# Kernel tuning notes

Measured on AMD Instinct MI355X. Metric: run time of the kernel, lower is better.

## Reference

```python
import jax, jax.numpy as jnp
import numpy as np

N_LVL = 127.0   # 8-bit symmetric: 2**(8-1) - 1
BN_EPS = 1e-5
PATCH = 16


def quant_act(x):
    """Per-tensor 8-bit symmetric quant-dequant (HAWQ-style QuantAct, dynamic range)."""
    scale = jnp.max(jnp.abs(x)) / N_LVL
    xq = jnp.clip(jnp.round(x / scale), -N_LVL, N_LVL) * scale
    return xq, scale


def setup_inputs() -> dict:
    key = jax.random.key(0)
    k0, k1, k2, k3, k4 = jax.random.split(key, 5)
    B, C, H = 128, 3, 224
    dim = 768
    x = jax.random.normal(k0, (B, C, H, H), jnp.float32)
    W = jax.random.normal(k1, (dim, C, PATCH, PATCH), jnp.float32) * 0.02
    b = jax.random.normal(k2, (dim,), jnp.float32) * 0.02
    gamma = jnp.ones((dim,), jnp.float32)
    beta = jnp.zeros((dim,), jnp.float32)
    run_mean = jax.random.normal(k3, (dim,), jnp.float32) * 0.1
    run_var = jax.random.uniform(k4, (dim,), jnp.float32, 0.5, 1.5)
    return {"x": x, "W": W, "b": b, "gamma": gamma, "beta": beta,
            "run_mean": run_mean, "run_var": run_var}


def reference(x, W, b, gamma, beta, run_mean, run_var):
    # --- quant_input ---
    x_q, pre_s = quant_act(x)                                   # [B,3,224,224], scalar
    # --- QuantConv2d: per-out-channel 8-bit symmetric weight quant ---
    w_scale = jnp.max(jnp.abs(W), axis=(1, 2, 3), keepdims=True) / N_LVL  # [dim,1,1,1]
    w_int = jnp.round(W / w_scale)
    x_int = x_q / pre_s                                         # integer-valued activations
    comb_s = w_scale[:, 0, 0, 0] * pre_s                        # [dim] conv output scale
    b_int = jnp.round(b / comb_s)
    y = jax.lax.conv_general_dilated(
        x_int, w_int, window_strides=(PATCH, PATCH), padding='VALID',
        dimension_numbers=('NCHW', 'OIHW', 'NCHW'))             # [B,768,14,14]
    y = (y + b_int[None, :, None, None]) * comb_s[None, :, None, None]
    # --- quant_act_conv ---
    y, _ = quant_act(y)
    # --- GELU (torch nn.GELU default: exact erf) ---
    y = jax.nn.gelu(y, approximate=False)
    # --- qact1 ---
    y, _ = quant_act(y)
    # --- BatchNorm2d (eval mode, running stats) ---
    inv = gamma / jnp.sqrt(run_var + BN_EPS)
    y = y * inv[None, :, None, None] + (beta - run_mean * inv)[None, :, None, None]
    # --- qact2 ---
    y, act_scale = quant_act(y)
    return y, act_scale
```

## Files before the change

kernel.cpp:

```cpp
#include <hip/hip_runtime.h>

#define TOT   19267584
#define MROWS 25088
#define KD    768
#define NPB   196
#define CHW   150528

typedef unsigned int uint;
typedef __attribute__((ext_vector_type(4))) int i32x4;

#define OFF_AQ   0ull
#define OFF_WQ   19267584ull
#define OFF_WSC  19857408ull
#define OFF_INV  19860480ull
#define OFF_SHF  19863552ull
#define OFF_PA   19866624ull
#define OFF_PB   19871328ull
#define OFF_CMN  19876032ull
#define OFF_CMX  19879104ull

__device__ __forceinline__ float wave_max(float v) {
#pragma unroll
  for (int off = 32; off > 0; off >>= 1) v = fmaxf(v, __shfl_xor(v, off));
  return v;
}

__device__ __forceinline__ float block_max(float v) {
  __shared__ float red[4];
  v = wave_max(v);
  __syncthreads();
  if ((threadIdx.x & 63) == 0) red[threadIdx.x >> 6] = v;
  __syncthreads();
  return fmaxf(fmaxf(red[0], red[1]), fmaxf(red[2], red[3]));
}

__global__ void k_maxabs(const float* __restrict__ x, float* __restrict__ pA) {
  const int i0 = blockIdx.x * 256 + threadIdx.x;
  const float4* x4 = (const float4*)x;
  float m = 0.f;
#pragma unroll
  for (int j = 0; j < 16; j += 4) {
    float4 a = x4[i0 + (j + 0) * 301056];
    float4 b = x4[i0 + (j + 1) * 301056];
    float4 c = x4[i0 + (j + 2) * 301056];
    float4 d = x4[i0 + (j + 3) * 301056];
    m = fmaxf(m, fmaxf(fmaxf(fabsf(a.x), fabsf(a.y)), fmaxf(fabsf(a.z), fabsf(a.w))));
    m = fmaxf(m, fmaxf(fmaxf(fabsf(b.x), fabsf(b.y)), fmaxf(fabsf(b.z), fabsf(b.w))));
    m = fmaxf(m, fmaxf(fmaxf(fabsf(c.x), fabsf(c.y)), fmaxf(fabsf(c.z), fabsf(c.w))));
    m = fmaxf(m, fmaxf(fmaxf(fabsf(d.x), fabsf(d.y)), fmaxf(fabsf(d.z), fabsf(d.w))));
  }
  float bm = block_max(m);
  if (threadIdx.x == 0) pA[blockIdx.x] = bm;
}

__global__ void k_wquant(const float* __restrict__ W, const float* __restrict__ gamma,
                         const float* __restrict__ beta, const float* __restrict__ rmean,
                         const float* __restrict__ rvar, signed char* __restrict__ wq,
                         float* __restrict__ wscale, float* __restrict__ inv_,
                         float* __restrict__ shf) {
  const int oc = blockIdx.x;
  const float* row = W + oc * KD;
  float m = 0.f;
  for (int k = threadIdx.x; k < KD; k += 256) m = fmaxf(m, fabsf(row[k]));
  const float ws_ = block_max(m) / 127.0f;
  for (int k = threadIdx.x; k < KD; k += 256)
    wq[oc * KD + k] = (signed char)(int)rintf(row[k] / ws_);
  if (threadIdx.x == 0) {
    wscale[oc] = ws_;
    float iv = gamma[oc] / sqrtf(rvar[oc] + 1e-5f);
    inv_[oc] = iv;
    shf[oc] = __fsub_rn(beta[oc], __fmul_rn(rmean[oc], iv));
  }
}

__global__ void k_im2col(const float* __restrict__ x, const float* __restrict__ pA,
                         signed char* __restrict__ aq) {
  float mm = 0.f;
  for (int i = threadIdx.x; i < 1176; i += 256) mm = fmaxf(mm, pA[i]);
  const float ps = block_max(mm) / 127.0f;
  const int u = blockIdx.x * 256 + threadIdx.x;
  const int p = u / 48, r = u - p * 48;
  const int c = r >> 4, kh = r & 15;
  const int b = p / NPB, pp = p - b * NPB;
  const int ph = pp / 14, pw = pp - ph * 14;
  const float* src = x + (((b * 3 + c) * 224 + ph * 16 + kh) * 224 + pw * 16);
  float4 v0 = *(const float4*)(src);
  float4 v1 = *(const float4*)(src + 4);
  float4 v2 = *(const float4*)(src + 8);
  float4 v3 = *(const float4*)(src + 12);
#define Q8(v) ((int)fminf(fmaxf(rintf((v) / ps), -127.f), 127.f) & 255)
  uint4 o;
  o.x = Q8(v0.x) | (Q8(v0.y) << 8) | (Q8(v0.z) << 16) | ((uint)Q8(v0.w) << 24);
  o.y = Q8(v1.x) | (Q8(v1.y) << 8) | (Q8(v1.z) << 16) | ((uint)Q8(v1.w) << 24);
  o.z = Q8(v2.x) | (Q8(v2.y) << 8) | (Q8(v2.z) << 16) | ((uint)Q8(v2.w) << 24);
  o.w = Q8(v3.x) | (Q8(v3.y) << 8) | (Q8(v3.z) << 16) | ((uint)Q8(v3.w) << 24);
#undef Q8
  *(uint4*)(aq + (size_t)p * KD + (r << 4)) = o;
}

__device__ __forceinline__ void gl_lds16(const void* g, void* l) {
  __builtin_amdgcn_global_load_lds((const __attribute__((address_space(1))) void*)g,
                                   (__attribute__((address_space(3))) void*)l, 16, 0, 0);
}

__global__ __launch_bounds__(256) void k_gemm(const signed char* __restrict__ aq,
                                              const signed char* __restrict__ wq,
                                              const float* __restrict__ bias,
                                              const float* __restrict__ wscale,
                                              const float* __restrict__ pA,
                                              float* __restrict__ y,
                                              float* __restrict__ pB) {
  __shared__ __align__(16) signed char lA[3][8192];
  __shared__ __align__(16) signed char lB[3][8192];
  const int tid = threadIdx.x, lane = tid & 63, wv = tid >> 6;
  const int bsw = (blockIdx.x & 7) * 147 + (blockIdx.x >> 3);
  const int bm = bsw / 6, bn = bsw - 6 * (bsw / 6);
  const int wr = wv >> 1, wc = wv & 1;

  const int ci0 = wv * 2, ci1 = wv * 2 + 1;
  const int rr0 = ci0 * 16 + (lane >> 2);
  const int rr1 = ci1 * 16 + (lane >> 2);
  const int bo = (((lane & 3) ^ ((lane >> 3) & 3)) << 4);
  const signed char* gA0 = aq + (size_t)(bm * 128 + rr0) * KD + bo;
  const signed char* gA1 = aq + (size_t)(bm * 128 + rr1) * KD + bo;
  const signed char* gB0 = wq + (size_t)(bn * 128 + rr0) * KD + bo;
  const signed char* gB1 = wq + (size_t)(bn * 128 + rr1) * KD + bo;

  i32x4 acc[4][4];
#pragma unroll
  for (int m = 0; m < 4; ++m)
#pragma unroll
    for (int n = 0; n < 4; ++n) acc[m][n] = (i32x4){0, 0, 0, 0};

  const int rbase = lane & 15;
  const int kg = (((lane >> 4) << 4)) ^ (((lane >> 1) & 3) << 4);

#define STAGE(T, B)                                   \
  {                                                   \
    const int kk_ = (T) * 64;                         \
    gl_lds16(gA0 + kk_, &lA[B][ci0 * 1024]);          \
    gl_lds16(gA1 + kk_, &lA[B][ci1 * 1024]);          \
    gl_lds16(gB0 + kk_, &lB[B][ci0 * 1024]);          \
    gl_lds16(gB1 + kk_, &lB[B][ci1 * 1024]);          \
  }

  STAGE(0, 0)
  STAGE(1, 1)
#pragma unroll
  for (int t = 0; t < 12; ++t) {
    if (t < 11) { asm volatile("s_waitcnt vmcnt(4)" ::: "memory"); }
    else        { asm volatile("s_waitcnt vmcnt(0)" ::: "memory"); }
    __builtin_amdgcn_s_barrier();
    __builtin_amdgcn_sched_barrier(0);
    const int b = t % 3;
    i32x4 af[4], bfr[4];
#pragma unroll
    for (int m = 0; m < 4; ++m)
      af[m] = *(const i32x4*)&lA[b][(wr * 64 + m * 16 + rbase) * 64 + kg];
#pragma unroll
    for (int n = 0; n < 4; ++n)
      bfr[n] = *(const i32x4*)&lB[b][(wc * 64 + n * 16 + rbase) * 64 + kg];
    if (t < 10) STAGE(t + 2, (t + 2) % 3)
#pragma unroll
    for (int m = 0; m < 4; ++m)
#pragma unroll
      for (int n = 0; n < 4; ++n)
        acc[m][n] = __builtin_amdgcn_mfma_i32_16x16x64_i8(af[m], bfr[n], acc[m][n], 0, 0, 0);
  }
#undef STAGE

  float mm = 0.f;
  for (int i = tid; i < 1176; i += 256) mm = fmaxf(mm, pA[i]);
  const float ps = block_max(mm) / 127.0f;

  float lmax = 0.f;
  const int prow = (lane >> 4) << 2;
#pragma unroll
  for (int n = 0; n < 4; ++n) {
    const int oc = bn * 128 + wc * 64 + n * 16 + rbase;
    const float comb = wscale[oc] * ps;
    const float bint = rintf(bias[oc] / comb);
#pragma unroll
    for (int m = 0; m < 4; ++m) {
      const int p0 = bm * 128 + wr * 64 + m * 16 + prow;
      const int img = p0 / 196;
      const int q = p0 - img * 196;
      float4 o;
      o.x = ((float)acc[m][n][0] + bint) * comb;
      o.y = ((float)acc[m][n][1] + bint) * comb;
      o.z = ((float)acc[m][n][2] + bint) * comb;
      o.w = ((float)acc[m][n][3] + bint) * comb;
      lmax = fmaxf(lmax, fmaxf(fmaxf(fabsf(o.x), fabsf(o.y)), fmaxf(fabsf(o.z), fabsf(o.w))));
      *(float4*)(y + (size_t)img * CHW + (size_t)oc * 196 + q) = o;
    }
  }
  float bm_ = block_max(lmax);
  if (tid == 0) pB[blockIdx.x] = bm_;
}

__global__ void k_gelu_chan(const float* __restrict__ y, const float* __restrict__ pB,
                            signed char* __restrict__ k1, float* __restrict__ chmn,
                            float* __restrict__ chmx) {
  const int c = blockIdx.x;
  float mm = 0.f;
  for (int i = threadIdx.x; i < 1176; i += 256) mm = fmaxf(mm, pB[i]);
  const float s1 = block_max(mm) / 127.0f;
  __shared__ float tab[255];
  for (int t = threadIdx.x; t < 255; t += 256) {
    float y1 = (float)(t - 127) * s1;
    float e = erff(y1 * 0.70710678118654752f);
    tab[t] = (y1 * (e + 1.0f)) * 0.5f;
  }
  __syncthreads();
  float mn = 1e30f, mx = -1e30f;
  const float4* y4 = (const float4*)y;
  char4* k4 = (char4*)k1;
#define ADDR(u) ((size_t)((u) / 49) * (CHW / 4) + (size_t)c * 49 + ((u) - ((u) / 49) * 49))
#define PROC(v, a4)                                                        \
  {                                                                        \
    int ia = (int)fminf(fmaxf(rintf((v).x / s1), -127.f), 127.f);          \
    int ib = (int)fminf(fmaxf(rintf((v).y / s1), -127.f), 127.f);          \
    int ic = (int)fminf(fmaxf(rintf((v).z / s1), -127.f), 127.f);          \
    int id = (int)fminf(fmaxf(rintf((v).w / s1), -127.f), 127.f);          \
    char4 kk;                                                              \
    kk.x = (signed char)ia; kk.y = (signed char)ib;                        \
    kk.z = (signed char)ic; kk.w = (signed char)id;                        \
    k4[a4] = kk;                                                           \
    float ga = tab[ia + 127], gb = tab[ib + 127];                          \
    float gc = tab[ic + 127], gd = tab[id + 127];                          \
    mn = fminf(mn, fminf(fminf(ga, gb), fminf(gc, gd)));                   \
    mx = fmaxf(mx, fmaxf(fmaxf(ga, gb), fmaxf(gc, gd)));                   \
  }
  for (int r = 0; r < 6; ++r) {
    const int u0 = threadIdx.x + r * 1024;
    const size_t a0 = ADDR(u0), a1 = ADDR(u0 + 256), a2 = ADDR(u0 + 512), a3 = ADDR(u0 + 768);
    float4 v0 = y4[a0];
    float4 v1 = y4[a1];
    float4 v2 = y4[a2];
    float4 v3 = y4[a3];
    PROC(v0, a0) PROC(v1, a1) PROC(v2, a2) PROC(v3, a3)
  }
  if (threadIdx.x < 128) {
    const int u = 6144 + threadIdx.x;
    const size_t a = ADDR(u);
    float4 v = y4[a];
    PROC(v, a)
  }
#undef PROC
#undef ADDR
  __shared__ float rmn[4], rmx[4];
#pragma unroll
  for (int off = 32; off > 0; off >>= 1) {
    mn = fminf(mn, __shfl_xor(mn, off));
    mx = fmaxf(mx, __shfl_xor(mx, off));
  }
  const int lane = threadIdx.x & 63, wvx = threadIdx.x >> 6;
  if (lane == 0) { rmn[wvx] = mn; rmx[wvx] = mx; }
  __syncthreads();
  if (threadIdx.x == 0) {
    chmn[c] = fminf(fminf(rmn[0], rmn[1]), fminf(rmn[2], rmn[3]));
    chmx[c] = fmaxf(fmaxf(rmx[0], rmx[1]), fmaxf(rmx[2], rmx[3]));
  }
}

__global__ void k_final(const signed char* __restrict__ k1, const float* __restrict__ pB,
                        const float* __restrict__ chmn, const float* __restrict__ chmx,
                        const float* __restrict__ inv_, const float* __restrict__ shf,
                        float* __restrict__ out) {
  float mm = 0.f;
  for (int i = threadIdx.x; i < 1176; i += 256) mm = fmaxf(mm, pB[i]);
  const float s1 = block_max(mm) / 127.0f;
  float m2 = 0.f;
  for (int c = threadIdx.x; c < 768; c += 256)
    m2 = fmaxf(m2, fmaxf(fabsf(chmn[c]), fabsf(chmx[c])));
  const float s2 = block_max(m2) / 127.0f;
  float m4 = 0.f;
  for (int c = threadIdx.x; c < 768; c += 256) {
    float iv = inv_[c], sh = shf[c];
    float a = fminf(fmaxf(rintf(chmn[c] / s2), -127.f), 127.f) * s2;
    float b = fminf(fmaxf(rintf(chmx[c] / s2), -127.f), 127.f) * s2;
    float ya = __fadd_rn(__fmul_rn(a, iv), sh);
    float yb = __fadd_rn(__fmul_rn(b, iv), sh);
    m4 = fmaxf(m4, fmaxf(fabsf(ya), fabsf(yb)));
  }
  const float s3 = block_max(m4) / 127.0f;

  __shared__ float tab[255];
  for (int t = threadIdx.x; t < 255; t += 256) {
    float y1 = (float)(t - 127) * s1;
    float e = erff(y1 * 0.70710678118654752f);
    float y2 = (y1 * (e + 1.0f)) * 0.5f;
    float q2 = fminf(fmaxf(rintf(y2 / s2), -127.f), 127.f);
    tab[t] = q2 * s2;
  }
  __syncthreads();
  const int i = blockIdx.x * 256 + threadIdx.x;
  const char4* k4 = (const char4*)k1;
  char4 a0 = k4[i];
  char4 a1 = k4[i + 1204224];
  char4 a2 = k4[i + 2 * 1204224];
  char4 a3 = k4[i + 3 * 1204224];
  float4* out4 = (float4*)out;
#define FIN(kk, idx)                                                       \
  {                                                                        \
    int c = ((idx) / 49) % 768;                                            \
    float iv = inv_[c], sh = shf[c];                                       \
    float fa = __fadd_rn(__fmul_rn(tab[kk.x + 127], iv), sh);              \
    float fb = __fadd_rn(__fmul_rn(tab[kk.y + 127], iv), sh);              \
    float fc = __fadd_rn(__fmul_rn(tab[kk.z + 127], iv), sh);              \
    float fd = __fadd_rn(__fmul_rn(tab[kk.w + 127], iv), sh);              \
    float4 o;                                                              \
    o.x = fminf(fmaxf(rintf(fa / s3), -127.f), 127.f) * s3;                \
    o.y = fminf(fmaxf(rintf(fb / s3), -127.f), 127.f) * s3;                \
    o.z = fminf(fmaxf(rintf(fc / s3), -127.f), 127.f) * s3;                \
    o.w = fminf(fmaxf(rintf(fd / s3), -127.f), 127.f) * s3;                \
    out4[idx] = o;                                                         \
  }
  FIN(a0, i)
  FIN(a1, i + 1204224)
  FIN(a2, i + 2 * 1204224)
  FIN(a3, i + 3 * 1204224)
#undef FIN
  if (blockIdx.x == 0 && threadIdx.x == 0) out[TOT] = s3;
}

extern "C" void kernel_launch(void* const* d_in, const int* in_sizes, int n_in,
                              void* d_out, int out_size, void* d_ws, size_t ws_size,
                              hipStream_t stream) {
  const float* x     = (const float*)d_in[0];
  const float* W     = (const float*)d_in[1];
  const float* bias  = (const float*)d_in[2];
  const float* gamma = (const float*)d_in[3];
  const float* beta  = (const float*)d_in[4];
  const float* rmean = (const float*)d_in[5];
  const float* rvar  = (const float*)d_in[6];
  float* out = (float*)d_out;
  char* ws = (char*)d_ws;

  signed char* aq  = (signed char*)(ws + OFF_AQ);
  signed char* wq  = (signed char*)(ws + OFF_WQ);
  float* wsc  = (float*)(ws + OFF_WSC);
  float* inv_ = (float*)(ws + OFF_INV);
  float* shf  = (float*)(ws + OFF_SHF);
  float* pA   = (float*)(ws + OFF_PA);
  float* pB   = (float*)(ws + OFF_PB);
  float* cmn  = (float*)(ws + OFF_CMN);
  float* cmx  = (float*)(ws + OFF_CMX);
  signed char* k1 = (signed char*)(ws + OFF_AQ);

  k_maxabs<<<1176, 256, 0, stream>>>(x, pA);
  k_wquant<<<768, 256, 0, stream>>>(W, gamma, beta, rmean, rvar, wq, wsc, inv_, shf);
  k_im2col<<<4704, 256, 0, stream>>>(x, pA, aq);
  k_gemm<<<1176, 256, 0, stream>>>(aq, wq, bias, wsc, pA, out, pB);
  k_gelu_chan<<<768, 256, 0, stream>>>(out, pB, k1, cmn, cmx);
  k_final<<<4704, 256, 0, stream>>>(k1, pB, cmn, cmx, inv_, shf, out);
}
```

Before: 125.6 us.

## Merge prologue kernels, halve GEMM M-tile, split per-channel GELU blocks

The input max-abs and weight-quant kernels become one launch with block-index dispatch, which saves a launch and lets the two run side by side. The GEMM tile shrinks from 128x128 to 64x128, giving 2352 blocks from one shared LDS buffer of three stages, to even out work across CUs. Each GELU per-channel block is split into two halves over the batch, with per-half min/max combined in the final kernel. Each GEMM block now does less MFMA work per byte loaded and the partial-max arrays get longer, so reuse drops and per-block overhead rises.

```diff
diff --git a/kernel.cpp b/kernel.cpp
--- a/kernel.cpp
+++ b/kernel.cpp
@@ -16,8 +16,8 @@
 #define OFF_SHF  19863552ull
 #define OFF_PA   19866624ull
 #define OFF_PB   19871328ull
-#define OFF_CMN  19876032ull
-#define OFF_CMX  19879104ull
+#define OFF_CMN  19880736ull
+#define OFF_CMX  19886880ull
 
 __device__ __forceinline__ float wave_max(float v) {
 #pragma unroll
@@ -34,42 +34,43 @@
   return fmaxf(fmaxf(red[0], red[1]), fmaxf(red[2], red[3]));
 }
 
-__global__ void k_maxabs(const float* __restrict__ x, float* __restrict__ pA) {
-  const int i0 = blockIdx.x * 256 + threadIdx.x;
-  const float4* x4 = (const float4*)x;
-  float m = 0.f;
-#pragma unroll
-  for (int j = 0; j < 16; j += 4) {
-    float4 a = x4[i0 + (j + 0) * 301056];
-    float4 b = x4[i0 + (j + 1) * 301056];
-    float4 c = x4[i0 + (j + 2) * 301056];
-    float4 d = x4[i0 + (j + 3) * 301056];
-    m = fmaxf(m, fmaxf(fmaxf(fabsf(a.x), fabsf(a.y)), fmaxf(fabsf(a.z), fabsf(a.w))));
-    m = fmaxf(m, fmaxf(fmaxf(fabsf(b.x), fabsf(b.y)), fmaxf(fabsf(b.z), fabsf(b.w))));
-    m = fmaxf(m, fmaxf(fmaxf(fabsf(c.x), fabsf(c.y)), fmaxf(fabsf(c.z), fabsf(c.w))));
-    m = fmaxf(m, fmaxf(fmaxf(fabsf(d.x), fabsf(d.y)), fmaxf(fabsf(d.z), fabsf(d.w))));
-  }
-  float bm = block_max(m);
-  if (threadIdx.x == 0) pA[blockIdx.x] = bm;
-}
-
-__global__ void k_wquant(const float* __restrict__ W, const float* __restrict__ gamma,
+__global__ void k_max_wq(const float* __restrict__ x, float* __restrict__ pA,
+                         const float* __restrict__ W, const float* __restrict__ gamma,
                          const float* __restrict__ beta, const float* __restrict__ rmean,
                          const float* __restrict__ rvar, signed char* __restrict__ wq,
                          float* __restrict__ wscale, float* __restrict__ inv_,
                          float* __restrict__ shf) {
-  const int oc = blockIdx.x;
-  const float* row = W + oc * KD;
-  float m = 0.f;
-  for (int k = threadIdx.x; k < KD; k += 256) m = fmaxf(m, fabsf(row[k]));
-  const float ws_ = block_max(m) / 127.0f;
-  for (int k = threadIdx.x; k < KD; k += 256)
-    wq[oc * KD + k] = (signed char)(int)rintf(row[k] / ws_);
-  if (threadIdx.x == 0) {
-    wscale[oc] = ws_;
-    float iv = gamma[oc] / sqrtf(rvar[oc] + 1e-5f);
-    inv_[oc] = iv;
-    shf[oc] = __fsub_rn(beta[oc], __fmul_rn(rmean[oc], iv));
+  if (blockIdx.x < 1176) {
+    const int i0 = blockIdx.x * 256 + threadIdx.x;
+    const float4* x4 = (const float4*)x;
+    float m = 0.f;
+#pragma unroll
+    for (int j = 0; j < 16; j += 4) {
+      float4 a = x4[i0 + (j + 0) * 301056];
+      float4 b = x4[i0 + (j + 1) * 301056];
+      float4 c = x4[i0 + (j + 2) * 301056];
+      float4 d = x4[i0 + (j + 3) * 301056];
+      m = fmaxf(m, fmaxf(fmaxf(fabsf(a.x), fabsf(a.y)), fmaxf(fabsf(a.z), fabsf(a.w))));
+      m = fmaxf(m, fmaxf(fmaxf(fabsf(b.x), fabsf(b.y)), fmaxf(fabsf(b.z), fabsf(b.w))));
+      m = fmaxf(m, fmaxf(fmaxf(fabsf(c.x), fabsf(c.y)), fmaxf(fabsf(c.z), fabsf(c.w))));
+      m = fmaxf(m, fmaxf(fmaxf(fabsf(d.x), fabsf(d.y)), fmaxf(fabsf(d.z), fabsf(d.w))));
+    }
+    float bm = block_max(m);
+    if (threadIdx.x == 0) pA[blockIdx.x] = bm;
+  } else {
+    const int oc = blockIdx.x - 1176;
+    const float* row = W + oc * KD;
+    float m = 0.f;
+    for (int k = threadIdx.x; k < KD; k += 256) m = fmaxf(m, fabsf(row[k]));
+    const float ws_ = block_max(m) / 127.0f;
+    for (int k = threadIdx.x; k < KD; k += 256)
+      wq[oc * KD + k] = (signed char)(int)rintf(row[k] / ws_);
+    if (threadIdx.x == 0) {
+      wscale[oc] = ws_;
+      float iv = gamma[oc] / sqrtf(rvar[oc] + 1e-5f);
+      inv_[oc] = iv;
+      shf[oc] = __fsub_rn(beta[oc], __fmul_rn(rmean[oc], iv));
+    }
   }
 }
 
@@ -110,59 +111,57 @@
                                               const float* __restrict__ pA,
                                               float* __restrict__ y,
                                               float* __restrict__ pB) {
-  __shared__ __align__(16) signed char lA[3][8192];
-  __shared__ __align__(16) signed char lB[3][8192];
+  __shared__ __align__(16) signed char L[3][12288];
   const int tid = threadIdx.x, lane = tid & 63, wv = tid >> 6;
-  const int bsw = (blockIdx.x & 7) * 147 + (blockIdx.x >> 3);
+  const int bsw = (blockIdx.x & 7) * 294 + (blockIdx.x >> 3);
   const int bm = bsw / 6, bn = bsw - 6 * (bsw / 6);
   const int wr = wv >> 1, wc = wv & 1;
 
-  const int ci0 = wv * 2, ci1 = wv * 2 + 1;
-  const int rr0 = ci0 * 16 + (lane >> 2);
-  const int rr1 = ci1 * 16 + (lane >> 2);
   const int bo = (((lane & 3) ^ ((lane >> 3) & 3)) << 4);
-  const signed char* gA0 = aq + (size_t)(bm * 128 + rr0) * KD + bo;
-  const signed char* gA1 = aq + (size_t)(bm * 128 + rr1) * KD + bo;
-  const signed char* gB0 = wq + (size_t)(bn * 128 + rr0) * KD + bo;
-  const signed char* gB1 = wq + (size_t)(bn * 128 + rr1) * KD + bo;
-
-  i32x4 acc[4][4];
-#pragma unroll
-  for (int m = 0; m < 4; ++m)
+#define SRC(c) ((c) < 4 ? aq + (size_t)(bm * 64 + (c) * 16 + (lane >> 2)) * KD + bo \
+                        : wq + (size_t)(bn * 128 + ((c) - 4) * 16 + (lane >> 2)) * KD + bo)
+  const int c0 = wv * 3, c1 = wv * 3 + 1, c2 = wv * 3 + 2;
+  const signed char* g0 = SRC(c0);
+  const signed char* g1 = SRC(c1);
+  const signed char* g2 = SRC(c2);
+#undef SRC
+
+  i32x4 acc[2][4];
+#pragma unroll
+  for (int m = 0; m < 2; ++m)
 #pragma unroll
     for (int n = 0; n < 4; ++n) acc[m][n] = (i32x4){0, 0, 0, 0};
 
   const int rbase = lane & 15;
-  const int kg = (((lane >> 4) << 4)) ^ (((lane >> 1) & 3) << 4);
+  const int kg = ((lane >> 4) << 4) ^ (((lane >> 1) & 3) << 4);
 
 #define STAGE(T, B)                                   \
   {                                                   \
     const int kk_ = (T) * 64;                         \
-    gl_lds16(gA0 + kk_, &lA[B][ci0 * 1024]);          \
-    gl_lds16(gA1 + kk_, &lA[B][ci1 * 1024]);          \
-    gl_lds16(gB0 + kk_, &lB[B][ci0 * 1024]);          \
-    gl_lds16(gB1 + kk_, &lB[B][ci1 * 1024]);          \
+    gl_lds16(g0 + kk_, &L[B][c0 * 1024]);             \
+    gl_lds16(g1 + kk_, &L[B][c1 * 1024]);             \
+    gl_lds16(g2 + kk_, &L[B][c2 * 1024]);             \
   }
 
   STAGE(0, 0)
   STAGE(1, 1)
 #pragma unroll
   for (int t = 0; t < 12; ++t) {
-    if (t < 11) { asm volatile("s_waitcnt vmcnt(4)" ::: "memory"); }
+    if (t < 11) { asm volatile("s_waitcnt vmcnt(3)" ::: "memory"); }
     else        { asm volatile("s_waitcnt vmcnt(0)" ::: "memory"); }
     __builtin_amdgcn_s_barrier();
     __builtin_amdgcn_sched_barrier(0);
     const int b = t % 3;
-    i32x4 af[4], bfr[4];
-#pragma unroll
-    for (int m = 0; m < 4; ++m)
-      af[m] = *(const i32x4*)&lA[b][(wr * 64 + m * 16 + rbase) * 64 + kg];
+    i32x4 af[2], bfr[4];
+#pragma unroll
+    for (int m = 0; m < 2; ++m)
+      af[m] = *(const i32x4*)&L[b][(wr * 32 + m * 16 + rbase) * 64 + kg];
 #pragma unroll
     for (int n = 0; n < 4; ++n)
-      bfr[n] = *(const i32x4*)&lB[b][(wc * 64 + n * 16 + rbase) * 64 + kg];
+      bfr[n] = *(const i32x4*)&L[b][4096 + (wc * 64 + n * 16 + rbase) * 64 + kg];
     if (t < 10) STAGE(t + 2, (t + 2) % 3)
 #pragma unroll
-    for (int m = 0; m < 4; ++m)
+    for (int m = 0; m < 2; ++m)
 #pragma unroll
       for (int n = 0; n < 4; ++n)
         acc[m][n] = __builtin_amdgcn_mfma_i32_16x16x64_i8(af[m], bfr[n], acc[m][n], 0, 0, 0);
@@ -181,8 +180,8 @@
     const float comb = wscale[oc] * ps;
     const float bint = rintf(bias[oc] / comb);
 #pragma unroll
-    for (int m = 0; m < 4; ++m) {
-      const int p0 = bm * 128 + wr * 64 + m * 16 + prow;
+    for (int m = 0; m < 2; ++m) {
+      const int p0 = bm * 64 + wr * 32 + m * 16 + prow;
       const int img = p0 / 196;
       const int q = p0 - img * 196;
       float4 o;
@@ -199,11 +198,11 @@
 }
 
 __global__ void k_gelu_chan(const float* __restrict__ y, const float* __restrict__ pB,
-                            signed char* __restrict__ k1, float* __restrict__ chmn,
-                            float* __restrict__ chmx) {
-  const int c = blockIdx.x;
+                            signed char* __restrict__ k1, float* __restrict__ cmn2,
+                            float* __restrict__ cmx2) {
+  const int c = blockIdx.x >> 1, half = blockIdx.x & 1;
   float mm = 0.f;
-  for (int i = threadIdx.x; i < 1176; i += 256) mm = fmaxf(mm, pB[i]);
+  for (int i = threadIdx.x; i < 2352; i += 256) mm = fmaxf(mm, pB[i]);
   const float s1 = block_max(mm) / 127.0f;
   __shared__ float tab[255];
   for (int t = threadIdx.x; t < 255; t += 256) {
@@ -215,7 +214,7 @@
   float mn = 1e30f, mx = -1e30f;
   const float4* y4 = (const float4*)y;
   char4* k4 = (char4*)k1;
-#define ADDR(u) ((size_t)((u) / 49) * (CHW / 4) + (size_t)c * 49 + ((u) - ((u) / 49) * 49))
+#define ADDR(u) ((size_t)(half * 64 + (u) / 49) * (CHW / 4) + (size_t)c * 49 + ((u) - ((u) / 49) * 49))
 #define PROC(v, a4)                                                        \
   {                                                                        \
     int ia = (int)fminf(fmaxf(rintf((v).x / s1), -127.f), 127.f);          \
@@ -231,7 +230,7 @@
     mn = fminf(mn, fminf(fminf(ga, gb), fminf(gc, gd)));                   \
     mx = fmaxf(mx, fmaxf(fmaxf(ga, gb), fmaxf(gc, gd)));                   \
   }
-  for (int r = 0; r < 6; ++r) {
+  for (int r = 0; r < 3; ++r) {
     const int u0 = threadIdx.x + r * 1024;
     const size_t a0 = ADDR(u0), a1 = ADDR(u0 + 256), a2 = ADDR(u0 + 512), a3 = ADDR(u0 + 768);
     float4 v0 = y4[a0];
@@ -240,8 +239,8 @@
     float4 v3 = y4[a3];
     PROC(v0, a0) PROC(v1, a1) PROC(v2, a2) PROC(v3, a3)
   }
-  if (threadIdx.x < 128) {
-    const int u = 6144 + threadIdx.x;
+  if (threadIdx.x < 64) {
+    const int u = 3072 + threadIdx.x;
     const size_t a = ADDR(u);
     float4 v = y4[a];
     PROC(v, a)
@@ -258,27 +257,29 @@
   if (lane == 0) { rmn[wvx] = mn; rmx[wvx] = mx; }
   __syncthreads();
   if (threadIdx.x == 0) {
-    chmn[c] = fminf(fminf(rmn[0], rmn[1]), fminf(rmn[2], rmn[3]));
-    chmx[c] = fmaxf(fmaxf(rmx[0], rmx[1]), fmaxf(rmx[2], rmx[3]));
+    cmn2[blockIdx.x] = fminf(fminf(rmn[0], rmn[1]), fminf(rmn[2], rmn[3]));
+    cmx2[blockIdx.x] = fmaxf(fmaxf(rmx[0], rmx[1]), fmaxf(rmx[2], rmx[3]));
   }
 }
 
 __global__ void k_final(const signed char* __restrict__ k1, const float* __restrict__ pB,
-                        const float* __restrict__ chmn, const float* __restrict__ chmx,
+                        const float* __restrict__ cmn2, const float* __restrict__ cmx2,
                         const float* __restrict__ inv_, const float* __restrict__ shf,
                         float* __restrict__ out) {
   float mm = 0.f;
-  for (int i = threadIdx.x; i < 1176; i += 256) mm = fmaxf(mm, pB[i]);
+  for (int i = threadIdx.x; i < 2352; i += 256) mm = fmaxf(mm, pB[i]);
   const float s1 = block_max(mm) / 127.0f;
   float m2 = 0.f;
-  for (int c = threadIdx.x; c < 768; c += 256)
-    m2 = fmaxf(m2, fmaxf(fabsf(chmn[c]), fabsf(chmx[c])));
+  for (int i = threadIdx.x; i < 1536; i += 256)
+    m2 = fmaxf(m2, fmaxf(fabsf(cmn2[i]), fabsf(cmx2[i])));
   const float s2 = block_max(m2) / 127.0f;
   float m4 = 0.f;
   for (int c = threadIdx.x; c < 768; c += 256) {
+    float mn = fminf(cmn2[2 * c], cmn2[2 * c + 1]);
+    float mx = fmaxf(cmx2[2 * c], cmx2[2 * c + 1]);
     float iv = inv_[c], sh = shf[c];
-    float a = fminf(fmaxf(rintf(chmn[c] / s2), -127.f), 127.f) * s2;
-    float b = fminf(fmaxf(rintf(chmx[c] / s2), -127.f), 127.f) * s2;
+    float a = fminf(fmaxf(rintf(mn / s2), -127.f), 127.f) * s2;
+    float b = fminf(fmaxf(rintf(mx / s2), -127.f), 127.f) * s2;
     float ya = __fadd_rn(__fmul_rn(a, iv), sh);
     float yb = __fadd_rn(__fmul_rn(b, iv), sh);
     m4 = fmaxf(m4, fmaxf(fabsf(ya), fabsf(yb)));
@@ -344,14 +345,13 @@
   float* shf  = (float*)(ws + OFF_SHF);
   float* pA   = (float*)(ws + OFF_PA);
   float* pB   = (float*)(ws + OFF_PB);
-  float* cmn  = (float*)(ws + OFF_CMN);
-  float* cmx  = (float*)(ws + OFF_CMX);
+  float* cmn2 = (float*)(ws + OFF_CMN);
+  float* cmx2 = (float*)(ws + OFF_CMX);
   signed char* k1 = (signed char*)(ws + OFF_AQ);
 
-  k_maxabs<<<1176, 256, 0, stream>>>(x, pA);
-  k_wquant<<<768, 256, 0, stream>>>(W, gamma, beta, rmean, rvar, wq, wsc, inv_, shf);
+  k_max_wq<<<1944, 256, 0, stream>>>(x, pA, W, gamma, beta, rmean, rvar, wq, wsc, inv_, shf);
   k_im2col<<<4704, 256, 0, stream>>>(x, pA, aq);
-  k_gemm<<<1176, 256, 0, stream>>>(aq, wq, bias, wsc, pA, out, pB);
-  k_gelu_chan<<<768, 256, 0, stream>>>(out, pB, k1, cmn, cmx);
-  k_final<<<4704, 256, 0, stream>>>(k1, pB, cmn, cmx, inv_, shf, out);
-}
+  k_gemm<<<2352, 256, 0, stream>>>(aq, wq, bias, wsc, pA, out, pB);
+  k_gelu_chan<<<1536, 256, 0, stream>>>(out, pB, k1, cmn2, cmx2);
+  k_final<<<4704, 256, 0, stream>>>(k1, pB, cmn2, cmx2, inv_, shf, out);
+}
```

Result: no change. 128.0 us (+1.9%).
